# Optimization experiments

Hardware: AMD Instinct MI355X
Metric: run time of the kernel (lower is better)

Reference implementation:

```python
import jax, jax.numpy as jnp
import numpy as np

B, S, HID, H = 4, 2048, 1024, 16
D = HID // H  # head_dim = 64


def setup_inputs() -> dict:
    key = jax.random.key(0)
    ks = jax.random.split(key, 12)
    std = 0.02
    inp = {
        "q": jax.random.normal(ks[0], (B, S, HID), jnp.float32),
        "k": jax.random.normal(ks[1], (B, S, HID), jnp.float32),
        "v": jax.random.normal(ks[2], (B, S, HID), jnp.float32),
        # causal mask: True where attention is NOT allowed (masked_fill semantics)
        "attn_mask": jnp.broadcast_to(
            ~jnp.tril(jnp.ones((S, S), jnp.bool_)), (B, S, S)
        ),
        "Wq": jax.random.normal(ks[3], (HID, HID), jnp.float32) * std,
        "bq": jnp.zeros((HID,), jnp.float32),
        "Wk": jax.random.normal(ks[4], (HID, HID), jnp.float32) * std,
        "bk": jnp.zeros((HID,), jnp.float32),
        "Wv": jax.random.normal(ks[5], (HID, HID), jnp.float32) * std,
        "bv": jnp.zeros((HID,), jnp.float32),
        "Wo": jax.random.normal(ks[6], (HID, HID), jnp.float32) * std,
        "bo": jnp.zeros((HID,), jnp.float32),
    }
    return inp


def _split_heads(x):
    # [B, S, HID] -> [B, H, S, D]
    b, s, _ = x.shape
    return x.reshape(b, s, H, D).transpose(0, 2, 1, 3)


def reference(q, k, v, attn_mask, Wq, bq, Wk, bk, Wv, bv, Wo, bo):
    qh = _split_heads(q @ Wq.T + bq)  # [B,H,S,D]
    kh = _split_heads(k @ Wk.T + bk)
    vh = _split_heads(v @ Wv.T + bv)
    scale = 1.0 / jnp.sqrt(jnp.asarray(D, qh.dtype))
    scores = jnp.einsum("bhqd,bhkd->bhqk", qh, kh) * scale  # [B,H,S,S]
    neg = jnp.asarray(-1e9, scores.dtype)
    scores = jnp.where(attn_mask[:, None, :, :], neg, scores)
    attn = jax.nn.softmax(scores, axis=-1)
    ctx = jnp.einsum("bhqk,bhkd->bhqd", attn, vh)  # [B,H,S,D]
    ctx = ctx.transpose(0, 2, 1, 3).reshape(q.shape[0], q.shape[1], HID)
    return ctx @ Wo.T + bo
```

## Files before the change

### kernel.cpp

```cpp
#include <hip/hip_runtime.h>

typedef __attribute__((ext_vector_type(8))) short short8;
typedef __attribute__((ext_vector_type(4))) float f32x4;
typedef __attribute__((ext_vector_type(16))) float f32x16;

#define S_LEN 2048
#define HIDN  1024
#define NHEAD 16
#define DHEAD 64

__device__ __forceinline__ short f2bf(float x) {
    unsigned u = __float_as_uint(x);
    u += 0x7fffu + ((u >> 16) & 1u);
    return (short)(u >> 16);
}

typedef const __attribute__((address_space(1))) void* gas_ptr;
typedef __attribute__((address_space(3))) void* las_ptr;

__device__ __forceinline__ void gload_lds16(const void* g, void* l) {
    __builtin_amdgcn_global_load_lds((gas_ptr)g, (las_ptr)l, 16, 0, 0);
}

__device__ __forceinline__ unsigned cvtpk(float lo, float hi_) {
    unsigned r;
    asm("v_cvt_pk_bf16_f32 %0, %1, %2" : "=v"(r) : "v"(lo), "v"(hi_));
    return r;
}

__device__ __forceinline__ void plswap(unsigned& x, unsigned& y) {
    asm("v_permlane32_swap_b32 %0, %1" : "+&v"(x), "+&v"(y));
}

__device__ __forceinline__ short8 mk8(unsigned a, unsigned b, unsigned c, unsigned d) {
    union { unsigned u[4]; short8 s; } t;
    t.u[0] = a; t.u[1] = b; t.u[2] = c; t.u[3] = d;
    return t.s;
}

__global__ __launch_bounds__(256) void cvt_all(const float* __restrict__ q,
                                               const float* __restrict__ k,
                                               const float* __restrict__ v,
                                               const float* __restrict__ Wq,
                                               const float* __restrict__ Wk,
                                               const float* __restrict__ Wv,
                                               const float* __restrict__ Wo,
                                               short* __restrict__ qb,
                                               short* __restrict__ kb,
                                               short* __restrict__ vb,
                                               short* __restrict__ wqb,
                                               short* __restrict__ wkb,
                                               short* __restrict__ wvb,
                                               short* __restrict__ wob) {
    int bid = blockIdx.x;
    const float* in;
    short* out;
    int base;
    if (bid < 2048) {
        int wsel = bid >> 9;
        base = bid & 511;
        in  = wsel == 0 ? Wq  : wsel == 1 ? Wk  : wsel == 2 ? Wv  : Wo;
        out = wsel == 0 ? wqb : wsel == 1 ? wkb : wsel == 2 ? wvb : wob;
    } else if (bid < 6144)  { in = q; out = qb; base = bid - 2048; }
    else if (bid < 10240)   { in = k; out = kb; base = bid - 6144; }
    else                    { in = v; out = vb; base = bid - 10240; }
    int i = (base * 256 + threadIdx.x) * 8;
    float4 a = *(const float4*)(in + i);
    float4 b = *(const float4*)(in + i + 4);
    short8 o;
    o[0] = f2bf(a.x); o[1] = f2bf(a.y); o[2] = f2bf(a.z); o[3] = f2bf(a.w);
    o[4] = f2bf(b.x); o[5] = f2bf(b.y); o[6] = f2bf(b.z); o[7] = f2bf(b.w);
    *(short8*)(out + i) = o;
}

__device__ __forceinline__ void gemm_k64_db8(const short* A, const short* Wb,
                                             short* As0, short* As1,
                                             short* Bs0, short* Bs1,
                                             f32x4 acc[4][2], int m0, int n0) {
    int tid = threadIdx.x;
    int w = tid >> 6, l = tid & 63, g = l >> 4, r = l & 15;
    int wm = w >> 2, wn = w & 3;
    int r7 = r & 7;

    int s0 = w * 64 + l, s1 = s0 + 512;
    int row0 = s0 >> 3, src0 = (((s0 & 7) ^ (row0 & 7))) * 8;
    int row1 = s1 >> 3, src1 = (((s1 & 7) ^ (row1 & 7))) * 8;
    int d0 = s0 * 8, d1 = s1 * 8;

    gload_lds16(A + (size_t)(m0 + row0) * HIDN + src0, As0 + d0);
    gload_lds16(A + (size_t)(m0 + row1) * HIDN + src1, As0 + d1);
    gload_lds16(Wb + (size_t)(n0 + row0) * HIDN + src0, Bs0 + d0);
    gload_lds16(Wb + (size_t)(n0 + row1) * HIDN + src1, Bs0 + d1);
    __syncthreads();

    for (int kt = 0; kt < HIDN / 64; ++kt) {
        short* Asc = (kt & 1) ? As1 : As0;
        short* Bsc = (kt & 1) ? Bs1 : Bs0;
        short* Asn = (kt & 1) ? As0 : As1;
        short* Bsn = (kt & 1) ? Bs0 : Bs1;
        if (kt + 1 < HIDN / 64) {
            int kc = (kt + 1) * 64;
            gload_lds16(A + (size_t)(m0 + row0) * HIDN + kc + src0, Asn + d0);
            gload_lds16(A + (size_t)(m0 + row1) * HIDN + kc + src1, Asn + d1);
            gload_lds16(Wb + (size_t)(n0 + row0) * HIDN + kc + src0, Bsn + d0);
            gload_lds16(Wb + (size_t)(n0 + row1) * HIDN + kc + src1, Bsn + d1);
        }
        short8 af[4][2], bfr[2][2];
#pragma unroll
        for (int i = 0; i < 4; i++)
#pragma unroll
            for (int ks = 0; ks < 2; ks++)
                af[i][ks] = *(const short8*)(Asc + (wm * 64 + i * 16 + r) * 64 +
                                             ((((ks << 2) + g) ^ r7) << 3));
#pragma unroll
        for (int j = 0; j < 2; j++)
#pragma unroll
            for (int ks = 0; ks < 2; ks++)
                bfr[j][ks] = *(const short8*)(Bsc + (wn * 32 + j * 16 + r) * 64 +
                                              ((((ks << 2) + g) ^ r7) << 3));
        __builtin_amdgcn_s_setprio(1);
#pragma unroll
        for (int i = 0; i < 4; i++)
#pragma unroll
            for (int j = 0; j < 2; j++) {
                acc[i][j] = __builtin_amdgcn_mfma_f32_16x16x32_bf16(af[i][0], bfr[j][0], acc[i][j], 0, 0, 0);
                acc[i][j] = __builtin_amdgcn_mfma_f32_16x16x32_bf16(af[i][1], bfr[j][1], acc[i][j], 0, 0, 0);
            }
        __builtin_amdgcn_s_setprio(0);
        __syncthreads();
    }
}

__global__ __launch_bounds__(512) void gemm_qkv(const short* __restrict__ qb,
                                                const short* __restrict__ kb,
                                                const short* __restrict__ vb,
                                                const short* __restrict__ Wqb,
                                                const short* __restrict__ Wkb,
                                                const short* __restrict__ Wvb,
                                                const float* __restrict__ bq,
                                                const float* __restrict__ bk,
                                                const float* __restrict__ bv,
                                                short* __restrict__ Qh,
                                                short* __restrict__ Kh,
                                                short* __restrict__ VhT,
                                                float qscale) {
    int which = blockIdx.x >> 9;
    int bid = blockIdx.x & 511;
    const short* A = which == 0 ? qb : which == 1 ? kb : vb;
    const short* Wb = which == 0 ? Wqb : which == 1 ? Wkb : Wvb;
    const float* bias = which == 0 ? bq : which == 1 ? bk : bv;
    short* Out = which == 0 ? Qh : which == 1 ? Kh : VhT;
    float oscale = which == 0 ? qscale : 1.0f;
    int omode = which == 2 ? 1 : 0;

    int mt = bid & 63, nt = bid >> 6;
    int m0 = mt * 128, n0 = nt * 128;
    int tid = threadIdx.x;
    int w = tid >> 6, l = tid & 63, g = l >> 4, r = l & 15;
    int wm = w >> 2, wn = w & 3;

    __shared__ short As0[128 * 64], As1[128 * 64];
    __shared__ short Bs0[128 * 64], Bs1[128 * 64];

    f32x4 acc[4][2];
#pragma unroll
    for (int i = 0; i < 4; i++)
#pragma unroll
        for (int j = 0; j < 2; j++) acc[i][j] = (f32x4){0.f, 0.f, 0.f, 0.f};

    gemm_k64_db8(A, Wb, As0, As1, Bs0, Bs1, acc, m0, n0);

#pragma unroll
    for (int j = 0; j < 2; j++) {
        int n_g = n0 + wn * 32 + j * 16 + r;
        float bv2 = bias[n_g];
        int h = n_g >> 6, d = n_g & 63;
#pragma unroll
        for (int i = 0; i < 4; i++) {
#pragma unroll
            for (int rr = 0; rr < 4; rr++) {
                int m_g = m0 + wm * 64 + i * 16 + g * 4 + rr;
                float val = (acc[i][j][rr] + bv2) * oscale;
                int b = m_g >> 11, s = m_g & 2047;
                size_t idx = (omode == 0)
                    ? (((size_t)(b * NHEAD + h)) * S_LEN + s) * DHEAD + d
                    : (((size_t)(b * NHEAD + h)) * DHEAD + d) * S_LEN + s;
                Out[idx] = f2bf(val);
            }
        }
    }
}

__global__ __launch_bounds__(512) void gemm_out(const short* __restrict__ A,
                                                const short* __restrict__ Wb,
                                                const float* __restrict__ bias,
                                                float* __restrict__ Out) {
    int mt = blockIdx.x & 63, nt = blockIdx.x >> 6;
    int m0 = mt * 128, n0 = nt * 128;
    int tid = threadIdx.x;
    int w = tid >> 6, l = tid & 63, g = l >> 4, r = l & 15;
    int wm = w >> 2, wn = w & 3;

    __shared__ short As0[128 * 64], As1[128 * 64];
    __shared__ short Bs0[128 * 64], Bs1[128 * 64];

    f32x4 acc[4][2];
#pragma unroll
    for (int i = 0; i < 4; i++)
#pragma unroll
        for (int j = 0; j < 2; j++) acc[i][j] = (f32x4){0.f, 0.f, 0.f, 0.f};

    gemm_k64_db8(A, Wb, As0, As1, Bs0, Bs1, acc, m0, n0);

#pragma unroll
    for (int j = 0; j < 2; j++) {
        int n_g = n0 + wn * 32 + j * 16 + r;
        float bv = bias[n_g];
#pragma unroll
        for (int i = 0; i < 4; i++) {
#pragma unroll
            for (int rr = 0; rr < 4; rr++) {
                int m_g = m0 + wm * 64 + i * 16 + g * 4 + rr;
                Out[(size_t)m_g * HIDN + n_g] = acc[i][j][rr] + bv;
            }
        }
    }
}

__global__ __launch_bounds__(512) void attn_kernel(const short* __restrict__ Qh,
                                                   const short* __restrict__ Kh,
                                                   const short* __restrict__ VhT,
                                                   short* __restrict__ ctx) {
    int bid = blockIdx.x;
    int m = bid >> 8;
    int u = bid & 255;
    int q2 = u >> 6;
    int bh = ((u >> 3) & 7) * 8 + (u & 7);
    int j = m ? (7 - q2) : q2;
    int qtB = 15 - j;
    int tid = threadIdx.x;
    int w = tid >> 6, l = tid & 63;
    int ql = l & 31, hi = l >> 5;
    int wq = w & 3, grp = w >> 2;
    int qt = grp ? qtB : j;

    __shared__ short KV[2][2][64 * 64];

    const short* Qb = Qh + (size_t)bh * (S_LEN * DHEAD);
    const short* Kb = Kh + (size_t)bh * (S_LEN * DHEAD);
    const short* Vb = VhT + (size_t)bh * (DHEAD * S_LEN);

    int srow = tid >> 3;
    int scol = (tid & 7) * 8;
    int wo = srow * 64 + (scol ^ ((srow & 7) << 3));

    int r0 = ql, r1 = 32 + ql;
    int sw = (ql & 7) << 3;
    int ch = hi * 8;
    int b = bh >> 4, h = bh & 15;

    int q_g = qt * 128 + wq * 32 + ql;
    const short* qp = Qb + (size_t)q_g * DHEAD + hi * 8;
    short8 qf0 = *(const short8*)(qp);
    short8 qf1 = *(const short8*)(qp + 16);
    short8 qf2 = *(const short8*)(qp + 32);
    short8 qf3 = *(const short8*)(qp + 48);

    f32x16 accA, accB;
#pragma unroll
    for (int i = 0; i < 16; ++i) { accA[i] = 0.f; accB[i] = 0.f; }
    float lrun = 0.f;

    int ktp = (qt * 128 + wq * 32) >> 6;
    int nt = 2 * qtB + 2;

    {
        short8 k0 = *(const short8*)(Kb + srow * 64 + scol);
        short8 v0 = *(const short8*)(Vb + (size_t)srow * S_LEN + scol);
        *(short8*)(&KV[0][0][wo]) = k0;
        *(short8*)(&KV[0][1][wo]) = v0;
    }

    for (int kt = 0; kt < nt; ++kt) {
        __syncthreads();
        int cur = kt & 1;
        short8 pk0, pv0;
        bool pf = (kt + 1 < nt);
        if (pf) {
            pk0 = *(const short8*)(Kb + (kt + 1) * (64 * DHEAD) + srow * 64 + scol);
            pv0 = *(const short8*)(Vb + (size_t)srow * S_LEN + (kt + 1) * 64 + scol);
        }
        if (kt <= ktp) {
            const short* Ksb = &KV[cur][0][0];
            const short* Vsb = &KV[cur][1][0];
            f32x16 st0, st1;
#pragma unroll
            for (int i = 0; i < 16; ++i) { st0[i] = 0.f; st1[i] = 0.f; }
            {
                short8 kA, kB;
                kA = *(const short8*)(Ksb + r0 * 64 + ((0 + ch) ^ sw));
                kB = *(const short8*)(Ksb + r1 * 64 + ((0 + ch) ^ sw));
                __builtin_amdgcn_s_setprio(1);
                st0 = __builtin_amdgcn_mfma_f32_32x32x16_bf16(kA, qf0, st0, 0, 0, 0);
                st1 = __builtin_amdgcn_mfma_f32_32x32x16_bf16(kB, qf0, st1, 0, 0, 0);
                __builtin_amdgcn_s_setprio(0);
                kA = *(const short8*)(Ksb + r0 * 64 + ((16 + ch) ^ sw));
                kB = *(const short8*)(Ksb + r1 * 64 + ((16 + ch) ^ sw));
                __builtin_amdgcn_s_setprio(1);
                st0 = __builtin_amdgcn_mfma_f32_32x32x16_bf16(kA, qf1, st0, 0, 0, 0);
                st1 = __builtin_amdgcn_mfma_f32_32x32x16_bf16(kB, qf1, st1, 0, 0, 0);
                __builtin_amdgcn_s_setprio(0);
                kA = *(const short8*)(Ksb + r0 * 64 + ((32 + ch) ^ sw));
                kB = *(const short8*)(Ksb + r1 * 64 + ((32 + ch) ^ sw));
                __builtin_amdgcn_s_setprio(1);
                st0 = __builtin_amdgcn_mfma_f32_32x32x16_bf16(kA, qf2, st0, 0, 0, 0);
                st1 = __builtin_amdgcn_mfma_f32_32x32x16_bf16(kB, qf2, st1, 0, 0, 0);
                __builtin_amdgcn_s_setprio(0);
                kA = *(const short8*)(Ksb + r0 * 64 + ((48 + ch) ^ sw));
                kB = *(const short8*)(Ksb + r1 * 64 + ((48 + ch) ^ sw));
                __builtin_amdgcn_s_setprio(1);
                st0 = __builtin_amdgcn_mfma_f32_32x32x16_bf16(kA, qf3, st0, 0, 0, 0);
                st1 = __builtin_amdgcn_mfma_f32_32x32x16_bf16(kB, qf3, st1, 0, 0, 0);
                __builtin_amdgcn_s_setprio(0);
            }
            float p[32];
#pragma unroll
            for (int i = 0; i < 16; ++i) { p[i] = st0[i]; p[16 + i] = st1[i]; }
            if (kt == ktp) {
#pragma unroll
                for (int i = 0; i < 32; ++i) {
                    int kl = (i & 3) + 8 * ((i >> 2) & 3) + 32 * (i >> 4) + 4 * hi;
                    if (kt * 64 + kl > q_g) p[i] = -1e30f;
                }
            }
#pragma unroll
            for (int i = 0; i < 32; ++i) p[i] = exp2f(p[i]);
            float t[16];
#pragma unroll
            for (int i = 0; i < 16; ++i) t[i] = p[i] + p[i + 16];
#pragma unroll
            for (int i = 0; i < 8; ++i) t[i] = t[i] + t[i + 8];
#pragma unroll
            for (int i = 0; i < 4; ++i) t[i] = t[i] + t[i + 4];
            float rs = (t[0] + t[1]) + (t[2] + t[3]);
            rs += __shfl_xor(rs, 32);
            lrun += rs;
            {
                unsigned u0 = cvtpk(p[0], p[1]);
                unsigned u1 = cvtpk(p[2], p[3]);
                unsigned u2 = cvtpk(p[4], p[5]);
                unsigned u3 = cvtpk(p[6], p[7]);
                plswap(u0, u2);
                plswap(u1, u3);
                short8 pfA = mk8(u0, u1, u2, u3);
                unsigned u4 = cvtpk(p[8], p[9]);
                unsigned u5 = cvtpk(p[10], p[11]);
                unsigned u6 = cvtpk(p[12], p[13]);
                unsigned u7 = cvtpk(p[14], p[15]);
                plswap(u4, u6);
                plswap(u5, u7);
                short8 pfB = mk8(u4, u5, u6, u7);
                short8 vA0 = *(const short8*)(Vsb + r0 * 64 + ((0 + ch) ^ sw));
                short8 vB0 = *(const short8*)(Vsb + r1 * 64 + ((0 + ch) ^ sw));
                short8 vA1 = *(const short8*)(Vsb + r0 * 64 + ((16 + ch) ^ sw));
                short8 vB1 = *(const short8*)(Vsb + r1 * 64 + ((16 + ch) ^ sw));
                __builtin_amdgcn_s_setprio(1);
                accA = __builtin_amdgcn_mfma_f32_32x32x16_bf16(vA0, pfA, accA, 0, 0, 0);
                accB = __builtin_amdgcn_mfma_f32_32x32x16_bf16(vB0, pfA, accB, 0, 0, 0);
                accA = __builtin_amdgcn_mfma_f32_32x32x16_bf16(vA1, pfB, accA, 0, 0, 0);
                accB = __builtin_amdgcn_mfma_f32_32x32x16_bf16(vB1, pfB, accB, 0, 0, 0);
                __builtin_amdgcn_s_setprio(0);
            }
            {
                unsigned u0 = cvtpk(p[16], p[17]);
                unsigned u1 = cvtpk(p[18], p[19]);
                unsigned u2 = cvtpk(p[20], p[21]);
                unsigned u3 = cvtpk(p[22], p[23]);
                plswap(u0, u2);
                plswap(u1, u3);
                short8 pfC = mk8(u0, u1, u2, u3);
                unsigned u4 = cvtpk(p[24], p[25]);
                unsigned u5 = cvtpk(p[26], p[27]);
                unsigned u6 = cvtpk(p[28], p[29]);
                unsigned u7 = cvtpk(p[30], p[31]);
                plswap(u4, u6);
                plswap(u5, u7);
                short8 pfD = mk8(u4, u5, u6, u7);
                short8 vA2 = *(const short8*)(Vsb + r0 * 64 + ((32 + ch) ^ sw));
                short8 vB2 = *(const short8*)(Vsb + r1 * 64 + ((32 + ch) ^ sw));
                short8 vA3 = *(const short8*)(Vsb + r0 * 64 + ((48 + ch) ^ sw));
                short8 vB3 = *(const short8*)(Vsb + r1 * 64 + ((48 + ch) ^ sw));
                __builtin_amdgcn_s_setprio(1);
                accA = __builtin_amdgcn_mfma_f32_32x32x16_bf16(vA2, pfC, accA, 0, 0, 0);
                accB = __builtin_amdgcn_mfma_f32_32x32x16_bf16(vB2, pfC, accB, 0, 0, 0);
                accA = __builtin_amdgcn_mfma_f32_32x32x16_bf16(vA3, pfD, accA, 0, 0, 0);
                accB = __builtin_amdgcn_mfma_f32_32x32x16_bf16(vB3, pfD, accB, 0, 0, 0);
                __builtin_amdgcn_s_setprio(0);
            }
        }
        if (pf) {
            int nb = (kt + 1) & 1;
            *(short8*)(&KV[nb][0][wo]) = pk0;
            *(short8*)(&KV[nb][1][wo]) = pv0;
        }
    }

    float inv = 1.0f / lrun;
    short* cb = ctx + ((size_t)(b * S_LEN + q_g)) * HIDN + h * DHEAD;
#pragma unroll
    for (int i = 0; i < 16; ++i) {
        int d0 = (i & 3) + 8 * (i >> 2) + 4 * hi;
        cb[d0] = f2bf(accA[i] * inv);
        cb[32 + d0] = f2bf(accB[i] * inv);
    }
}

extern "C" void kernel_launch(void* const* d_in, const int* in_sizes, int n_in,
                              void* d_out, int out_size, void* d_ws, size_t ws_size,
                              hipStream_t stream) {
    const float* q  = (const float*)d_in[0];
    const float* k  = (const float*)d_in[1];
    const float* v  = (const float*)d_in[2];
    const float* Wq = (const float*)d_in[4];
    const float* bq = (const float*)d_in[5];
    const float* Wk = (const float*)d_in[6];
    const float* bk = (const float*)d_in[7];
    const float* Wv = (const float*)d_in[8];
    const float* bv = (const float*)d_in[9];
    const float* Wo = (const float*)d_in[10];
    const float* bo = (const float*)d_in[11];

    char* ws = (char*)d_ws;
    const size_t ACT = (size_t)8192 * 1024 * 2;
    const size_t WSZ = (size_t)1024 * 1024 * 2;
    short* Qh  = (short*)(ws);
    short* Kh  = (short*)(ws + ACT);
    short* VhT = (short*)(ws + 2 * ACT);
    short* qb  = (short*)(ws + 3 * ACT);
    short* kb  = (short*)(ws + 4 * ACT);
    short* vb  = (short*)(ws + 5 * ACT);
    short* ctx = qb;
    short* Wqb = (short*)(ws + 6 * ACT);
    short* Wkb = (short*)(ws + 6 * ACT + WSZ);
    short* Wvb = (short*)(ws + 6 * ACT + 2 * WSZ);
    short* Wob = (short*)(ws + 6 * ACT + 3 * WSZ);

    cvt_all<<<14336, 256, 0, stream>>>(q, k, v, Wq, Wk, Wv, Wo,
                                       qb, kb, vb, Wqb, Wkb, Wvb, Wob);

    const float QSCALE = 0.125f * 1.44269504088896340736f;
    gemm_qkv<<<1536, 512, 0, stream>>>(qb, kb, vb, Wqb, Wkb, Wvb, bq, bk, bv,
                                       Qh, Kh, VhT, QSCALE);

    attn_kernel<<<512, 512, 0, stream>>>(Qh, Kh, VhT, ctx);

    gemm_out<<<512, 512, 0, stream>>>(ctx, Wob, bo, (float*)d_out);
}
```

Before: 178.8 us.

## Split KV range across two wave groups per query tile and merge partials

Each block now handles a single 128-row query tile instead of pairing a short and a long causal tile, and the launch doubles to 1024 blocks. The two 4-wave groups split the key range in half, each staging its own K/V tile in separate LDS regions. The groups then merge their unnormalized accumulators and row sums through shared memory before writing. This is a split-K (flash-decoding style) scheme that relies on the max-free exp2 softmax, so partials can simply be added. It aims to shorten the serial KV loop and improve load balance, at the cost of a merge step, an extra barrier per iteration and no more double buffering.

```diff
diff --git a/kernel.cpp b/kernel.cpp
--- a/kernel.cpp
+++ b/kernel.cpp
@@ -234,30 +234,35 @@
     int bid = blockIdx.x;
     int m = bid >> 8;
     int u = bid & 255;
-    int q2 = u >> 6;
+    int q4 = u >> 6;
     int bh = ((u >> 3) & 7) * 8 + (u & 7);
-    int j = m ? (7 - q2) : q2;
-    int qtB = 15 - j;
+    int qt = (m == 0) ? q4 : (m == 1) ? (7 - q4) : (m == 2) ? (8 + q4) : (15 - q4);
     int tid = threadIdx.x;
     int w = tid >> 6, l = tid & 63;
     int ql = l & 31, hi = l >> 5;
     int wq = w & 3, grp = w >> 2;
-    int qt = grp ? qtB : j;
-
-    __shared__ short KV[2][2][64 * 64];
+
+    __align__(16) __shared__ char smem[34816];
+    short* KVb = (short*)smem + grp * 8192;
+    float* MG = (float*)smem;
 
     const short* Qb = Qh + (size_t)bh * (S_LEN * DHEAD);
     const short* Kb = Kh + (size_t)bh * (S_LEN * DHEAD);
     const short* Vb = VhT + (size_t)bh * (DHEAD * S_LEN);
 
-    int srow = tid >> 3;
-    int scol = (tid & 7) * 8;
-    int wo = srow * 64 + (scol ^ ((srow & 7) << 3));
+    int h = qt + 1;
+    int base = grp ? h : 0;
+
+    int tc = tid & 255;
+    int srow0 = tc >> 3, srow1 = srow0 + 32;
+    int scol = (tc & 7) * 8;
+    int wo0 = srow0 * 64 + (scol ^ ((srow0 & 7) << 3));
+    int wo1 = srow1 * 64 + (scol ^ ((srow1 & 7) << 3));
 
     int r0 = ql, r1 = 32 + ql;
     int sw = (ql & 7) << 3;
     int ch = hi * 8;
-    int b = bh >> 4, h = bh & 15;
+    int b = bh >> 4, hd = bh & 15;
 
     int q_g = qt * 128 + wq * 32 + ql;
     const short* qp = Qb + (size_t)q_g * DHEAD + hi * 8;
@@ -272,27 +277,30 @@
     float lrun = 0.f;
 
     int ktp = (qt * 128 + wq * 32) >> 6;
-    int nt = 2 * qtB + 2;
-
-    {
-        short8 k0 = *(const short8*)(Kb + srow * 64 + scol);
-        short8 v0 = *(const short8*)(Vb + (size_t)srow * S_LEN + scol);
-        *(short8*)(&KV[0][0][wo]) = k0;
-        *(short8*)(&KV[0][1][wo]) = v0;
-    }
-
-    for (int kt = 0; kt < nt; ++kt) {
+
+    short8 pk0 = *(const short8*)(Kb + (size_t)base * 64 * DHEAD + srow0 * 64 + scol);
+    short8 pk1 = *(const short8*)(Kb + (size_t)base * 64 * DHEAD + srow1 * 64 + scol);
+    short8 pv0 = *(const short8*)(Vb + (size_t)srow0 * S_LEN + base * 64 + scol);
+    short8 pv1 = *(const short8*)(Vb + (size_t)srow1 * S_LEN + base * 64 + scol);
+
+    for (int it = 0; it < h; ++it) {
         __syncthreads();
-        int cur = kt & 1;
-        short8 pk0, pv0;
-        bool pf = (kt + 1 < nt);
-        if (pf) {
-            pk0 = *(const short8*)(Kb + (kt + 1) * (64 * DHEAD) + srow * 64 + scol);
-            pv0 = *(const short8*)(Vb + (size_t)srow * S_LEN + (kt + 1) * 64 + scol);
-        }
-        if (kt <= ktp) {
-            const short* Ksb = &KV[cur][0][0];
-            const short* Vsb = &KV[cur][1][0];
+        *(short8*)(KVb + wo0) = pk0;
+        *(short8*)(KVb + wo1) = pk1;
+        *(short8*)(KVb + 4096 + wo0) = pv0;
+        *(short8*)(KVb + 4096 + wo1) = pv1;
+        __syncthreads();
+        int g = base + it;
+        if (it + 1 < h) {
+            int gn = g + 1;
+            pk0 = *(const short8*)(Kb + (size_t)gn * 64 * DHEAD + srow0 * 64 + scol);
+            pk1 = *(const short8*)(Kb + (size_t)gn * 64 * DHEAD + srow1 * 64 + scol);
+            pv0 = *(const short8*)(Vb + (size_t)srow0 * S_LEN + gn * 64 + scol);
+            pv1 = *(const short8*)(Vb + (size_t)srow1 * S_LEN + gn * 64 + scol);
+        }
+        if (g <= ktp) {
+            const short* Ksb = KVb;
+            const short* Vsb = KVb + 4096;
             f32x16 st0, st1;
 #pragma unroll
             for (int i = 0; i < 16; ++i) { st0[i] = 0.f; st1[i] = 0.f; }
@@ -326,11 +334,11 @@
             float p[32];
 #pragma unroll
             for (int i = 0; i < 16; ++i) { p[i] = st0[i]; p[16 + i] = st1[i]; }
-            if (kt == ktp) {
+            if (g == ktp) {
 #pragma unroll
                 for (int i = 0; i < 32; ++i) {
                     int kl = (i & 3) + 8 * ((i >> 2) & 3) + 32 * (i >> 4) + 4 * hi;
-                    if (kt * 64 + kl > q_g) p[i] = -1e30f;
+                    if (g * 64 + kl > q_g) p[i] = -1e30f;
                 }
             }
 #pragma unroll
@@ -398,20 +406,29 @@
                 __builtin_amdgcn_s_setprio(0);
             }
         }
-        if (pf) {
-            int nb = (kt + 1) & 1;
-            *(short8*)(&KV[nb][0][wo]) = pk0;
-            *(short8*)(&KV[nb][1][wo]) = pv0;
-        }
-    }
-
-    float inv = 1.0f / lrun;
-    short* cb = ctx + ((size_t)(b * S_LEN + q_g)) * HIDN + h * DHEAD;
-#pragma unroll
-    for (int i = 0; i < 16; ++i) {
-        int d0 = (i & 3) + 8 * (i >> 2) + 4 * hi;
-        cb[d0] = f2bf(accA[i] * inv);
-        cb[32 + d0] = f2bf(accB[i] * inv);
+    }
+
+    __syncthreads();
+    if (grp == 1) {
+        float* mg = MG + ((wq << 6) + l) * 34;
+#pragma unroll
+        for (int i = 0; i < 16; ++i) { mg[i] = accA[i]; mg[16 + i] = accB[i]; }
+        mg[32] = lrun;
+    }
+    __syncthreads();
+    if (grp == 0) {
+        float* mg = MG + ((wq << 6) + l) * 34;
+#pragma unroll
+        for (int i = 0; i < 16; ++i) { accA[i] += mg[i]; accB[i] += mg[16 + i]; }
+        lrun += mg[32];
+        float inv = 1.0f / lrun;
+        short* cb = ctx + ((size_t)(b * S_LEN + q_g)) * HIDN + hd * DHEAD;
+#pragma unroll
+        for (int i = 0; i < 16; ++i) {
+            int d0 = (i & 3) + 8 * (i >> 2) + 4 * hi;
+            cb[d0] = f2bf(accA[i] * inv);
+            cb[32 + d0] = f2bf(accB[i] * inv);
+        }
     }
 }
 
@@ -452,7 +469,7 @@
     gemm_qkv<<<1536, 512, 0, stream>>>(qb, kb, vb, Wqb, Wkb, Wvb, bq, bk, bv,
                                        Qh, Kh, VhT, QSCALE);
 
-    attn_kernel<<<512, 512, 0, stream>>>(Qh, Kh, VhT, ctx);
+    attn_kernel<<<1024, 512, 0, stream>>>(Qh, Kh, VhT, ctx);
 
     gemm_out<<<512, 512, 0, stream>>>(ctx, Wob, bo, (float*)d_out);
 }
```

Result: slower. 194.2 us (+8.6%).
